# Kernel optimization log

Measured on AMD Instinct MI355X. Metric: run time of the kernel, lower is better.

The kernel has to match this reference:

```python
import jax, jax.numpy as jnp
import numpy as np

T, D, H, E, K = 8192, 512, 1024, 16, 2  # tokens, d_model, d_hidden, num_expert, top_k


def setup_inputs() -> dict:
    key = jax.random.key(0)
    ks = jax.random.split(key, 4)
    return {
        "x": jax.random.normal(ks[0], (T, D), jnp.float32),
        "Wg": jax.random.normal(ks[1], (D, E), jnp.float32) * (D ** -0.5),
        "bg": jnp.zeros((E,), jnp.float32),
        "W1": jax.random.normal(ks[2], (E, D, H), jnp.float32) * (D ** -0.5),
        "b1": jnp.zeros((E, H), jnp.float32),
        "W2": jax.random.normal(ks[3], (E, H, D), jnp.float32) * (H ** -0.5),
        "b2": jnp.zeros((E, D), jnp.float32),
    }


def _moe(x, Wg, bg, W1, b1, W2, b2):
    # NaiveGate: linear -> top-k -> softmax over the k selected logits
    logits = x @ Wg + bg                              # [T, E]
    top_val, top_idx = jax.lax.top_k(logits, K)       # [T, K]
    score = jax.nn.softmax(top_val, axis=-1)          # [T, K]
    # Dispatch + per-expert MLP + combine. Mathematically identical to the
    # scatter/grouped-GEMM/gather: for each expert, the per-token combine
    # weight is the gate score if the token routed there, else 0.
    out = jnp.zeros_like(x)
    for e in range(E):  # fixed small loop over structurally distinct experts
        h = jax.nn.gelu(x @ W1[e] + b1[e], approximate=False)  # [T, H]
        y = h @ W2[e] + b2[e]                                   # [T, D]
        w_e = jnp.sum(jnp.where(top_idx == e, score, 0.0), axis=-1)  # [T]
        out = out + w_e[:, None] * y
    return out


def reference(x, Wg, bg, W1, b1, W2, b2):
    return _moe(x, Wg, bg, W1, b1, W2, b2)
```

## Files before the change

### kernel.cpp

```cpp
#include <hip/hip_runtime.h>
#include <hip/hip_bf16.h>
#include <math.h>

#define TT 8192
#define DD 512
#define HH 1024
#define EE 16
#define NSLOT 18432
#define MAXTILES 144
#define BM 128
#define RETRYCAP 1024

typedef __attribute__((ext_vector_type(8))) short bf16x8;
typedef __attribute__((ext_vector_type(8))) unsigned short u16x8;
typedef __attribute__((ext_vector_type(4))) float f32x4;

__device__ __forceinline__ unsigned short f2bf(float f) {
  union { float f; unsigned u; } v; v.f = f;
  unsigned r = v.u + 0x7fffu + ((v.u >> 16) & 1u);
  return (unsigned short)(r >> 16);
}

__device__ __forceinline__ float bf2f(unsigned short u) {
  union { unsigned u; float f; } v; v.u = ((unsigned)u) << 16;
  return v.f;
}

__device__ __forceinline__ void gload16(const void* g, void* l) {
  __builtin_amdgcn_global_load_lds(
      (const __attribute__((address_space(1))) unsigned int*)g,
      (__attribute__((address_space(3))) unsigned int*)l, 16, 0, 0);
}

__device__ __forceinline__ float gelu_f(float v) {
  float s = fabsf(v) * 0.70710678118654752f;
  float t = 1.0f / (1.0f + 0.3275911f * s);
  float poly = t * (0.254829592f +
              t * (-0.284496736f +
              t * (1.421413741f +
              t * (-1.453152027f +
              t * 1.061405429f))));
  float erfa = 1.0f - poly * __expf(-s * s);
  float erfv = (v >= 0.f) ? erfa : -erfa;
  return 0.5f * v * (1.0f + erfv);
}

__device__ __forceinline__ int tile_decode(const int* __restrict__ counts,
                                           int mt, int* e_out, int* row0_out) {
  int off = 0, rem = mt;
#pragma unroll
  for (int q = 0; q < EE; q++) {
    int tl = (counts[q] + BM - 1) / BM;
    if (rem < tl) { *e_out = q; *row0_out = off + rem * BM; return 1; }
    rem -= tl;
    off += tl * BM;
  }
  return 0;
}

__global__ __launch_bounds__(256) void transpose_cv_kernel(
    const float* __restrict__ W1, const float* __restrict__ W2,
    unsigned short* __restrict__ w1t, unsigned short* __restrict__ w2t) {
  __shared__ unsigned short t[64][68];
  int bid = blockIdx.x;
  int tid = threadIdx.x;
  const float* src;
  unsigned short* dst;
  int R, C, c0, r0;
  if (bid < 2048) {
    int cx = bid & 15, ry = (bid >> 4) & 7, mat = bid >> 7;
    src = W1 + (size_t)mat * DD * HH; dst = w1t + (size_t)mat * DD * HH;
    R = DD; C = HH; c0 = cx * 64; r0 = ry * 64;
  } else {
    int b = bid - 2048;
    int cx = b & 7, ry = (b >> 3) & 15, mat = b >> 7;
    src = W2 + (size_t)mat * DD * HH; dst = w2t + (size_t)mat * DD * HH;
    R = HH; C = DD; c0 = cx * 64; r0 = ry * 64;
  }
#pragma unroll
  for (int p = 0; p < 4; p++) {
    int r = tid >> 2;
    int c4 = (tid & 3) + p * 4;
    float4 v = *(const float4*)(src + (size_t)(r0 + r) * C + c0 + c4 * 4);
    t[c4 * 4 + 0][r] = f2bf(v.x);
    t[c4 * 4 + 1][r] = f2bf(v.y);
    t[c4 * 4 + 2][r] = f2bf(v.z);
    t[c4 * 4 + 3][r] = f2bf(v.w);
  }
  __syncthreads();
#pragma unroll
  for (int p = 0; p < 4; p++) {
    int oc = (tid >> 4) + p * 16;
    int ch = tid & 15;
    ushort4 v = *(ushort4*)(&t[oc][ch * 4]);
    *(ushort4*)(dst + (size_t)(c0 + oc) * R + r0 + ch * 4) = v;
  }
}

__global__ __launch_bounds__(256) void gate_mfma_kernel(
    const float* __restrict__ x, const float* __restrict__ Wg,
    const float* __restrict__ bg, unsigned short* __restrict__ xb,
    int* __restrict__ gate_e, float* __restrict__ gate_w,
    int* __restrict__ counts, int* __restrict__ nretry,
    int* __restrict__ retry) {
  __shared__ __align__(16) unsigned short As[128][40];
  __shared__ int cnt_s[EE];
  int tid = threadIdx.x;
  int lane = tid & 63;
  int wave = tid >> 6;
  int tok0 = blockIdx.x * 128;
  if (tid < EE) cnt_s[tid] = 0;
  int e = lane & 15;
  int kb = (lane >> 4) * 8;
  bf16x8 bfrag[16];
#pragma unroll
  for (int ks = 0; ks < 16; ks++) {
    int kbase = ks * 32 + kb;
#pragma unroll
    for (int j = 0; j < 8; j++)
      bfrag[ks][j] = (short)f2bf(Wg[(kbase + j) * EE + e]);
  }
  float bge = bg[e];
  f32x4 acc[2];
  {
    f32x4 z = {0.f, 0.f, 0.f, 0.f};
    acc[0] = z; acc[1] = z;
  }
  int srow = tid >> 1;
  int sc0 = (tid & 1) * 16;
  const float* xrow = x + (size_t)(tok0 + srow) * DD + sc0;
  unsigned short* xbrow = xb + (size_t)(tok0 + srow) * DD + sc0;
  for (int ks = 0; ks < 16; ks++) {
    int k0 = ks * 32;
    __syncthreads();
    float4 v0 = *(const float4*)(xrow + k0);
    float4 v1 = *(const float4*)(xrow + k0 + 4);
    float4 v2 = *(const float4*)(xrow + k0 + 8);
    float4 v3 = *(const float4*)(xrow + k0 + 12);
    u16x8 w0, w1;
    w0[0] = f2bf(v0.x); w0[1] = f2bf(v0.y); w0[2] = f2bf(v0.z); w0[3] = f2bf(v0.w);
    w0[4] = f2bf(v1.x); w0[5] = f2bf(v1.y); w0[6] = f2bf(v1.z); w0[7] = f2bf(v1.w);
    w1[0] = f2bf(v2.x); w1[1] = f2bf(v2.y); w1[2] = f2bf(v2.z); w1[3] = f2bf(v2.w);
    w1[4] = f2bf(v3.x); w1[5] = f2bf(v3.y); w1[6] = f2bf(v3.z); w1[7] = f2bf(v3.w);
    *(u16x8*)(xbrow + k0) = w0;
    *(u16x8*)(xbrow + k0 + 8) = w1;
    *(u16x8*)(&As[srow][sc0]) = w0;
    *(u16x8*)(&As[srow][sc0 + 8]) = w1;
    __syncthreads();
    bf16x8 a0 = *(const bf16x8*)(&As[wave * 32 + (lane & 15)][kb]);
    bf16x8 a1 = *(const bf16x8*)(&As[wave * 32 + 16 + (lane & 15)][kb]);
    acc[0] = __builtin_amdgcn_mfma_f32_16x16x32_bf16(a0, bfrag[ks], acc[0], 0, 0, 0);
    acc[1] = __builtin_amdgcn_mfma_f32_16x16x32_bf16(a1, bfrag[ks], acc[1], 0, 0, 0);
  }
#pragma unroll
  for (int m = 0; m < 2; m++) {
#pragma unroll
    for (int r = 0; r < 4; r++) {
      float lf = acc[m][r] + bge;
      float v1 = -1e30f, v2 = -1e30f, v3 = -1e30f;
      int i1 = 0, i2 = 0;
#pragma unroll
      for (int q = 0; q < EE; q++) {
        float v = __shfl(lf, (lane & 48) | q);
        if (v > v1) { v3 = v2; v2 = v1; i2 = i1; v1 = v; i1 = q; }
        else if (v > v2) { v3 = v2; v2 = v; i2 = q; }
        else if (v > v3) { v3 = v; }
      }
      if ((lane & 15) == 0) {
        int t2 = tok0 + wave * 32 + m * 16 + ((lane >> 4) << 2) + r;
        float p = expf(v2 - v1);
        float s = 1.0f / (1.0f + p);
        gate_e[t2 * 2] = i1;
        gate_e[t2 * 2 + 1] = i2;
        gate_w[t2 * 2] = s;
        gate_w[t2 * 2 + 1] = p * s;
        atomicAdd(&cnt_s[i1], 1);
        atomicAdd(&cnt_s[i2], 1);
        if (v2 - v3 < 0.02f) {
          int pos = atomicAdd(nretry, 1);
          if (pos < RETRYCAP) retry[pos] = t2;
        }
      }
    }
  }
  __syncthreads();
  if (tid < EE) atomicAdd(&counts[tid], cnt_s[tid]);
}

__global__ __launch_bounds__(256) void gatefix_kernel(
    const float* __restrict__ x, const float* __restrict__ Wg,
    const float* __restrict__ bg, const int* __restrict__ nretry,
    const int* __restrict__ retry, int* __restrict__ gate_e,
    float* __restrict__ gate_w, int* __restrict__ counts) {
  __shared__ float lg[16][17];
  __shared__ int toks[16];
  int tid = threadIdx.x;
  int sl = tid >> 4, e = tid & 15;
  int s = blockIdx.x * 16 + sl;
  int n = *nretry; if (n > RETRYCAP) n = RETRYCAP;
  int active = (s < n);
  int tok = 0;
  if (active) tok = retry[s];
  if (active) {
    const float* xr = x + (size_t)tok * DD;
    double a0 = 0.0, a1 = 0.0, a2 = 0.0, a3 = 0.0;
    for (int i = 0; i < DD / 4; i++) {
      a0 += (double)xr[i * 4 + 0] * (double)Wg[(i * 4 + 0) * EE + e];
      a1 += (double)xr[i * 4 + 1] * (double)Wg[(i * 4 + 1) * EE + e];
      a2 += (double)xr[i * 4 + 2] * (double)Wg[(i * 4 + 2) * EE + e];
      a3 += (double)xr[i * 4 + 3] * (double)Wg[(i * 4 + 3) * EE + e];
    }
    double acc = (a0 + a1) + (a2 + a3);
    lg[sl][e] = (float)(acc + (double)bg[e]);
    toks[sl] = tok;
  }
  __syncthreads();
  if (active && e == 0) {
    float v1 = -1e30f, v2 = -1e30f;
    int i1 = 0, i2 = 0;
#pragma unroll
    for (int q = 0; q < EE; q++) {
      float v = lg[sl][q];
      if (v > v1) { v2 = v1; i2 = i1; v1 = v; i1 = q; }
      else if (v > v2) { v2 = v; i2 = q; }
    }
    int t2 = toks[sl];
    int o1 = gate_e[t2 * 2], o2 = gate_e[t2 * 2 + 1];
    float p = expf(v2 - v1);
    float sc = 1.0f / (1.0f + p);
    gate_e[t2 * 2] = i1;
    gate_e[t2 * 2 + 1] = i2;
    gate_w[t2 * 2] = sc;
    gate_w[t2 * 2 + 1] = p * sc;
    if (o1 != i1 || o2 != i2) {
      atomicSub(&counts[o1], 1);
      atomicSub(&counts[o2], 1);
      atomicAdd(&counts[i1], 1);
      atomicAdd(&counts[i2], 1);
    }
  }
}

__global__ __launch_bounds__(256) void scatter_kernel(
    const int* __restrict__ gate_e, const float* __restrict__ gate_w,
    const int* __restrict__ counts, int* __restrict__ fill,
    int* __restrict__ slot_token, float* __restrict__ slot_w,
    int* __restrict__ slot_of) {
  __shared__ int lcnt[EE];
  __shared__ int lbase[EE];
  __shared__ int offs_s[EE];
  int tid = threadIdx.x;
  int t = blockIdx.x * 256 + tid;
  if (tid < EE) lcnt[tid] = 0;
  if (tid == 0) {
    int off = 0;
    for (int q = 0; q < EE; q++) {
      offs_s[q] = off;
      off += ((counts[q] + BM - 1) / BM) * BM;
    }
  }
  __syncthreads();
  int e0 = gate_e[t * 2], e1 = gate_e[t * 2 + 1];
  int p0 = atomicAdd(&lcnt[e0], 1);
  int p1 = atomicAdd(&lcnt[e1], 1);
  __syncthreads();
  if (tid < EE) lbase[tid] = atomicAdd(&fill[tid], lcnt[tid]);
  __syncthreads();
  int s0 = offs_s[e0] + lbase[e0] + p0;
  int s1 = offs_s[e1] + lbase[e1] + p1;
  slot_token[s0] = t;
  slot_w[s0] = gate_w[t * 2];
  slot_of[t * 2] = s0;
  slot_token[s1] = t;
  slot_w[s1] = gate_w[t * 2 + 1];
  slot_of[t * 2 + 1] = s1;
}

__global__ __launch_bounds__(256) void gemm1_kernel(
    const unsigned short* __restrict__ xb, const unsigned short* __restrict__ w1t,
    const float* __restrict__ b1, const int* __restrict__ slot_token,
    const int* __restrict__ counts, unsigned short* __restrict__ hb) {
  int e, row0;
  if (!tile_decode(counts, blockIdx.y, &e, &row0)) return;
  int n0 = blockIdx.x * 128;
  __shared__ unsigned short As[3][128][32];
  __shared__ unsigned short Bs[3][128][32];
  int tid = threadIdx.x;
  int lane = tid & 63;
  int wave = tid >> 6;
  int wm = wave >> 1, wn = wave & 1;
  int ra = tid >> 2, c = tid & 3;
  int tok_a = slot_token[row0 + ra]; if (tok_a < 0) tok_a = 0;
  int tok_b = slot_token[row0 + ra + 64]; if (tok_b < 0) tok_b = 0;
  const unsigned short* wbase = w1t + ((size_t)e * HH * DD);
  const unsigned short* gA0 = xb + (size_t)tok_a * DD + c * 8;
  const unsigned short* gA1 = xb + (size_t)tok_b * DD + c * 8;
  const unsigned short* gB0 = wbase + (size_t)(n0 + ra) * DD + c * 8;
  const unsigned short* gB1 = wbase + (size_t)(n0 + ra + 64) * DD + c * 8;
  f32x4 acc[4][4];
#pragma unroll
  for (int m = 0; m < 4; m++)
#pragma unroll
    for (int n = 0; n < 4; n++) {
      f32x4 z = {0.f, 0.f, 0.f, 0.f};
      acc[m][n] = z;
    }
  const int NK = DD / 32;
#pragma unroll
  for (int p = 0; p < 2; p++) {
    int kj = p * 32;
    gload16(gA0 + kj, &As[p][ra][c * 8]);
    gload16(gA1 + kj, &As[p][ra + 64][c * 8]);
    gload16(gB0 + kj, &Bs[p][ra][c * 8]);
    gload16(gB1 + kj, &Bs[p][ra + 64][c * 8]);
  }
  for (int kk = 0; kk < NK; kk++) {
    int cur = kk % 3;
    if (kk + 2 < NK) {
      int k2 = (kk + 2) * 32;
      int nx = (kk + 2) % 3;
      gload16(gA0 + k2, &As[nx][ra][c * 8]);
      gload16(gA1 + k2, &As[nx][ra + 64][c * 8]);
      gload16(gB0 + k2, &Bs[nx][ra][c * 8]);
      gload16(gB1 + k2, &Bs[nx][ra + 64][c * 8]);
      asm volatile("s_waitcnt vmcnt(8)" ::: "memory");
    } else if (kk + 1 < NK) {
      asm volatile("s_waitcnt vmcnt(4)" ::: "memory");
    } else {
      asm volatile("s_waitcnt vmcnt(0)" ::: "memory");
    }
    __builtin_amdgcn_s_barrier();
    bf16x8 a[4], b[4];
#pragma unroll
    for (int m = 0; m < 4; m++)
      a[m] = *(const bf16x8*)(&As[cur][wm * 64 + m * 16 + (lane & 15)][(lane >> 4) * 8]);
#pragma unroll
    for (int n = 0; n < 4; n++)
      b[n] = *(const bf16x8*)(&Bs[cur][wn * 64 + n * 16 + (lane & 15)][(lane >> 4) * 8]);
#pragma unroll
    for (int m = 0; m < 4; m++)
#pragma unroll
      for (int n = 0; n < 4; n++)
        acc[m][n] = __builtin_amdgcn_mfma_f32_16x16x32_bf16(a[m], b[n], acc[m][n], 0, 0, 0);
    asm volatile("" ::: "memory");
    __builtin_amdgcn_s_barrier();
  }
  const float* b1e = b1 + (size_t)e * HH;
#pragma unroll
  for (int m = 0; m < 4; m++) {
#pragma unroll
    for (int r = 0; r < 4; r++) {
      int slot = row0 + wm * 64 + m * 16 + ((lane >> 4) << 2) + r;
      unsigned short* hrow = hb + (size_t)slot * HH;
#pragma unroll
      for (int n = 0; n < 4; n++) {
        int hc = n0 + wn * 64 + n * 16 + (lane & 15);
        float v = acc[m][n][r] + b1e[hc];
        hrow[hc] = f2bf(gelu_f(v));
      }
    }
  }
}

template <int USE_Y>
__global__ __launch_bounds__(256) void gemm2_kernel(
    const unsigned short* __restrict__ hb, const unsigned short* __restrict__ w2t,
    const float* __restrict__ b2, const int* __restrict__ slot_token,
    const float* __restrict__ slot_w, const int* __restrict__ counts,
    unsigned short* __restrict__ yw, float* __restrict__ out) {
  int e, row0;
  if (!tile_decode(counts, blockIdx.y, &e, &row0)) return;
  int n0 = blockIdx.x * 128;
  __shared__ unsigned short As[3][128][32];
  __shared__ unsigned short Bs[3][128][32];
  int tid = threadIdx.x;
  int lane = tid & 63;
  int wave = tid >> 6;
  int wm = wave >> 1, wn = wave & 1;
  int ra = tid >> 2, c = tid & 3;
  const unsigned short* wbase = w2t + ((size_t)e * DD * HH);
  const unsigned short* gA0 = hb + (size_t)(row0 + ra) * HH + c * 8;
  const unsigned short* gA1 = hb + (size_t)(row0 + ra + 64) * HH + c * 8;
  const unsigned short* gB0 = wbase + (size_t)(n0 + ra) * HH + c * 8;
  const unsigned short* gB1 = wbase + (size_t)(n0 + ra + 64) * HH + c * 8;
  f32x4 acc[4][4];
#pragma unroll
  for (int m = 0; m < 4; m++)
#pragma unroll
    for (int n = 0; n < 4; n++) {
      f32x4 z = {0.f, 0.f, 0.f, 0.f};
      acc[m][n] = z;
    }
  const int NK = HH / 32;
#pragma unroll
  for (int p = 0; p < 2; p++) {
    int kj = p * 32;
    gload16(gA0 + kj, &As[p][ra][c * 8]);
    gload16(gA1 + kj, &As[p][ra + 64][c * 8]);
    gload16(gB0 + kj, &Bs[p][ra][c * 8]);
    gload16(gB1 + kj, &Bs[p][ra + 64][c * 8]);
  }
  for (int kk = 0; kk < NK; kk++) {
    int cur = kk % 3;
    if (kk + 2 < NK) {
      int k2 = (kk + 2) * 32;
      int nx = (kk + 2) % 3;
      gload16(gA0 + k2, &As[nx][ra][c * 8]);
      gload16(gA1 + k2, &As[nx][ra + 64][c * 8]);
      gload16(gB0 + k2, &Bs[nx][ra][c * 8]);
      gload16(gB1 + k2, &Bs[nx][ra + 64][c * 8]);
      asm volatile("s_waitcnt vmcnt(8)" ::: "memory");
    } else if (kk + 1 < NK) {
      asm volatile("s_waitcnt vmcnt(4)" ::: "memory");
    } else {
      asm volatile("s_waitcnt vmcnt(0)" ::: "memory");
    }
    __builtin_amdgcn_s_barrier();
    bf16x8 a[4], b[4];
#pragma unroll
    for (int m = 0; m < 4; m++)
      a[m] = *(const bf16x8*)(&As[cur][wm * 64 + m * 16 + (lane & 15)][(lane >> 4) * 8]);
#pragma unroll
    for (int n = 0; n < 4; n++)
      b[n] = *(const bf16x8*)(&Bs[cur][wn * 64 + n * 16 + (lane & 15)][(lane >> 4) * 8]);
#pragma unroll
    for (int m = 0; m < 4; m++)
#pragma unroll
      for (int n = 0; n < 4; n++)
        acc[m][n] = __builtin_amdgcn_mfma_f32_16x16x32_bf16(a[m], b[n], acc[m][n], 0, 0, 0);
    asm volatile("" ::: "memory");
    __builtin_amdgcn_s_barrier();
  }
  const float* b2e = b2 + (size_t)e * DD;
#pragma unroll
  for (int m = 0; m < 4; m++) {
#pragma unroll
    for (int r = 0; r < 4; r++) {
      int slot = row0 + wm * 64 + m * 16 + ((lane >> 4) << 2) + r;
      if (USE_Y) {
        float w = slot_w[slot];
        unsigned short* yrow = yw + (size_t)slot * DD;
#pragma unroll
        for (int n = 0; n < 4; n++) {
          int dc = n0 + wn * 64 + n * 16 + (lane & 15);
          yrow[dc] = f2bf(w * (acc[m][n][r] + b2e[dc]));
        }
      } else {
        int tok = slot_token[slot];
        if (tok >= 0) {
          float w = slot_w[slot];
          float* orow = out + (size_t)tok * DD;
#pragma unroll
          for (int n = 0; n < 4; n++) {
            int dc = n0 + wn * 64 + n * 16 + (lane & 15);
            float v = acc[m][n][r] + b2e[dc];
            atomicAdd(&orow[dc], w * v);
          }
        }
      }
    }
  }
}

__global__ __launch_bounds__(256) void combine_kernel(
    const unsigned short* __restrict__ yw, const int* __restrict__ slot_of,
    float* __restrict__ out) {
  int gid = blockIdx.x * 256 + threadIdx.x;
  int t = gid >> 6;
  int d0 = (gid & 63) * 8;
  int s1 = slot_of[t * 2], s2 = slot_of[t * 2 + 1];
  const ushort4* p1 = (const ushort4*)(yw + (size_t)s1 * DD + d0);
  const ushort4* p2 = (const ushort4*)(yw + (size_t)s2 * DD + d0);
  ushort4 a0 = p1[0], a1 = p1[1];
  ushort4 b0 = p2[0], b1 = p2[1];
  float4 o0, o1;
  o0.x = bf2f(a0.x) + bf2f(b0.x);
  o0.y = bf2f(a0.y) + bf2f(b0.y);
  o0.z = bf2f(a0.z) + bf2f(b0.z);
  o0.w = bf2f(a0.w) + bf2f(b0.w);
  o1.x = bf2f(a1.x) + bf2f(b1.x);
  o1.y = bf2f(a1.y) + bf2f(b1.y);
  o1.z = bf2f(a1.z) + bf2f(b1.z);
  o1.w = bf2f(a1.w) + bf2f(b1.w);
  float* orow = out + (size_t)t * DD + d0;
  ((float4*)orow)[0] = o0;
  ((float4*)orow)[1] = o1;
}

extern "C" void kernel_launch(void* const* d_in, const int* in_sizes, int n_in,
                              void* d_out, int out_size, void* d_ws, size_t ws_size,
                              hipStream_t stream) {
  const float* x  = (const float*)d_in[0];
  const float* Wg = (const float*)d_in[1];
  const float* bg = (const float*)d_in[2];
  const float* W1 = (const float*)d_in[3];
  const float* b1 = (const float*)d_in[4];
  const float* W2 = (const float*)d_in[5];
  const float* b2 = (const float*)d_in[6];
  float* out = (float*)d_out;

  uint8_t* w = (uint8_t*)d_ws;
  size_t o = 0;
  unsigned short* xb  = (unsigned short*)(w + o); o += (size_t)TT * DD * 2;
  unsigned short* w1t = (unsigned short*)(w + o); o += (size_t)EE * DD * HH * 2;
  unsigned short* w2t = (unsigned short*)(w + o); o += (size_t)EE * DD * HH * 2;
  unsigned short* hb  = (unsigned short*)(w + o); o += (size_t)NSLOT * HH * 2;
  int*   slot_token = (int*)(w + o);   o += (size_t)NSLOT * 4;
  float* slot_w     = (float*)(w + o); o += (size_t)NSLOT * 4;
  int*   slot_of    = (int*)(w + o);   o += (size_t)TT * 2 * 4;
  int*   gate_e     = (int*)(w + o);   o += (size_t)TT * 2 * 4;
  float* gate_w     = (float*)(w + o); o += (size_t)TT * 2 * 4;
  int*   counts     = (int*)(w + o);   o += 64;
  int*   nretry     = (int*)(w + o);   o += 64;
  int*   fill       = (int*)(w + o);   o += 64;
  int*   retry      = (int*)(w + o);   o += RETRYCAP * 4;
  unsigned short* yw = (unsigned short*)(w + o);
  size_t need_y = o + (size_t)NSLOT * DD * 2;
  int use_y = (ws_size >= need_y);

  hipMemsetAsync(counts, 0, 192, stream);
  hipMemsetAsync(slot_token, 0xFF, (size_t)NSLOT * 4, stream);
  if (!use_y) hipMemsetAsync(d_out, 0, (size_t)TT * DD * 4, stream);

  transpose_cv_kernel<<<4096, 256, 0, stream>>>(W1, W2, w1t, w2t);
  gate_mfma_kernel<<<TT / 128, 256, 0, stream>>>(x, Wg, bg, xb, gate_e, gate_w,
                                                 counts, nretry, retry);
  gatefix_kernel<<<RETRYCAP / 16, 256, 0, stream>>>(x, Wg, bg, nretry, retry,
                                                    gate_e, gate_w, counts);
  scatter_kernel<<<TT / 256, 256, 0, stream>>>(gate_e, gate_w, counts, fill,
                                               slot_token, slot_w, slot_of);
  {
    dim3 g(HH / 128, MAXTILES);
    gemm1_kernel<<<g, 256, 0, stream>>>(xb, w1t, b1, slot_token, counts, hb);
  }
  {
    dim3 g(DD / 128, MAXTILES);
    if (use_y)
      gemm2_kernel<1><<<g, 256, 0, stream>>>(hb, w2t, b2, slot_token, slot_w,
                                             counts, yw, out);
    else
      gemm2_kernel<0><<<g, 256, 0, stream>>>(hb, w2t, b2, slot_token, slot_w,
                                             counts, yw, out);
  }
  if (use_y) {
    combine_kernel<<<TT * (DD / 8) / 256, 256, 0, stream>>>(yw, slot_of, out);
  }
}
```

Before: 177.4 us.

## Drop LDS staging in gate kernel and fill only padding slots in scatter

```diff
diff --git a/kernel.cpp b/kernel.cpp
--- a/kernel.cpp
+++ b/kernel.cpp
@@ -97,19 +97,19 @@
   }
 }
 
-__global__ __launch_bounds__(256) void gate_mfma_kernel(
+__global__ __launch_bounds__(128) void gate_mfma_kernel(
     const float* __restrict__ x, const float* __restrict__ Wg,
     const float* __restrict__ bg, unsigned short* __restrict__ xb,
     int* __restrict__ gate_e, float* __restrict__ gate_w,
     int* __restrict__ counts, int* __restrict__ nretry,
     int* __restrict__ retry) {
-  __shared__ __align__(16) unsigned short As[128][40];
   __shared__ int cnt_s[EE];
   int tid = threadIdx.x;
   int lane = tid & 63;
   int wave = tid >> 6;
-  int tok0 = blockIdx.x * 128;
+  int tok0 = blockIdx.x * 32 + wave * 16;
   if (tid < EE) cnt_s[tid] = 0;
+  __syncthreads();
   int e = lane & 15;
   int kb = (lane >> 4) * 8;
   bf16x8 bfrag[16];
@@ -121,65 +121,46 @@
       bfrag[ks][j] = (short)f2bf(Wg[(kbase + j) * EE + e]);
   }
   float bge = bg[e];
-  f32x4 acc[2];
-  {
-    f32x4 z = {0.f, 0.f, 0.f, 0.f};
-    acc[0] = z; acc[1] = z;
-  }
-  int srow = tid >> 1;
-  int sc0 = (tid & 1) * 16;
-  const float* xrow = x + (size_t)(tok0 + srow) * DD + sc0;
-  unsigned short* xbrow = xb + (size_t)(tok0 + srow) * DD + sc0;
+  f32x4 acc = {0.f, 0.f, 0.f, 0.f};
+  const float* xrow = x + (size_t)(tok0 + (lane & 15)) * DD + kb;
+  unsigned short* xbrow = xb + (size_t)(tok0 + (lane & 15)) * DD + kb;
+#pragma unroll 4
   for (int ks = 0; ks < 16; ks++) {
     int k0 = ks * 32;
-    __syncthreads();
     float4 v0 = *(const float4*)(xrow + k0);
     float4 v1 = *(const float4*)(xrow + k0 + 4);
-    float4 v2 = *(const float4*)(xrow + k0 + 8);
-    float4 v3 = *(const float4*)(xrow + k0 + 12);
-    u16x8 w0, w1;
+    u16x8 w0;
     w0[0] = f2bf(v0.x); w0[1] = f2bf(v0.y); w0[2] = f2bf(v0.z); w0[3] = f2bf(v0.w);
     w0[4] = f2bf(v1.x); w0[5] = f2bf(v1.y); w0[6] = f2bf(v1.z); w0[7] = f2bf(v1.w);
-    w1[0] = f2bf(v2.x); w1[1] = f2bf(v2.y); w1[2] = f2bf(v2.z); w1[3] = f2bf(v2.w);
-    w1[4] = f2bf(v3.x); w1[5] = f2bf(v3.y); w1[6] = f2bf(v3.z); w1[7] = f2bf(v3.w);
     *(u16x8*)(xbrow + k0) = w0;
-    *(u16x8*)(xbrow + k0 + 8) = w1;
-    *(u16x8*)(&As[srow][sc0]) = w0;
-    *(u16x8*)(&As[srow][sc0 + 8]) = w1;
-    __syncthreads();
-    bf16x8 a0 = *(const bf16x8*)(&As[wave * 32 + (lane & 15)][kb]);
-    bf16x8 a1 = *(const bf16x8*)(&As[wave * 32 + 16 + (lane & 15)][kb]);
-    acc[0] = __builtin_amdgcn_mfma_f32_16x16x32_bf16(a0, bfrag[ks], acc[0], 0, 0, 0);
-    acc[1] = __builtin_amdgcn_mfma_f32_16x16x32_bf16(a1, bfrag[ks], acc[1], 0, 0, 0);
-  }
-#pragma unroll
-  for (int m = 0; m < 2; m++) {
-#pragma unroll
-    for (int r = 0; r < 4; r++) {
-      float lf = acc[m][r] + bge;
-      float v1 = -1e30f, v2 = -1e30f, v3 = -1e30f;
-      int i1 = 0, i2 = 0;
-#pragma unroll
-      for (int q = 0; q < EE; q++) {
-        float v = __shfl(lf, (lane & 48) | q);
-        if (v > v1) { v3 = v2; v2 = v1; i2 = i1; v1 = v; i1 = q; }
-        else if (v > v2) { v3 = v2; v2 = v; i2 = q; }
-        else if (v > v3) { v3 = v; }
-      }
-      if ((lane & 15) == 0) {
-        int t2 = tok0 + wave * 32 + m * 16 + ((lane >> 4) << 2) + r;
-        float p = expf(v2 - v1);
-        float s = 1.0f / (1.0f + p);
-        gate_e[t2 * 2] = i1;
-        gate_e[t2 * 2 + 1] = i2;
-        gate_w[t2 * 2] = s;
-        gate_w[t2 * 2 + 1] = p * s;
-        atomicAdd(&cnt_s[i1], 1);
-        atomicAdd(&cnt_s[i2], 1);
-        if (v2 - v3 < 0.02f) {
-          int pos = atomicAdd(nretry, 1);
-          if (pos < RETRYCAP) retry[pos] = t2;
-        }
+    union { u16x8 u; bf16x8 b; } cv; cv.u = w0;
+    acc = __builtin_amdgcn_mfma_f32_16x16x32_bf16(cv.b, bfrag[ks], acc, 0, 0, 0);
+  }
+#pragma unroll
+  for (int r = 0; r < 4; r++) {
+    float lf = acc[r] + bge;
+    float v1 = -1e30f, v2 = -1e30f, v3 = -1e30f;
+    int i1 = 0, i2 = 0;
+#pragma unroll
+    for (int q = 0; q < EE; q++) {
+      float v = __shfl(lf, (lane & 48) | q);
+      if (v > v1) { v3 = v2; v2 = v1; i2 = i1; v1 = v; i1 = q; }
+      else if (v > v2) { v3 = v2; v2 = v; i2 = q; }
+      else if (v > v3) { v3 = v; }
+    }
+    if ((lane & 15) == 0) {
+      int t2 = tok0 + ((lane >> 4) << 2) + r;
+      float p = expf(v2 - v1);
+      float s = 1.0f / (1.0f + p);
+      gate_e[t2 * 2] = i1;
+      gate_e[t2 * 2 + 1] = i2;
+      gate_w[t2 * 2] = s;
+      gate_w[t2 * 2 + 1] = p * s;
+      atomicAdd(&cnt_s[i1], 1);
+      atomicAdd(&cnt_s[i2], 1);
+      if (v2 - v3 < 0.02f) {
+        int pos = atomicAdd(nretry, 1);
+        if (pos < RETRYCAP) retry[pos] = t2;
       }
     }
   }
@@ -260,6 +241,15 @@
     }
   }
   __syncthreads();
+  if (blockIdx.x == 0) {
+#pragma unroll
+    for (int q = 0; q < EE; q++) {
+      int cnt = counts[q];
+      int lim = ((cnt + BM - 1) / BM) * BM;
+      for (int p = cnt + tid; p < lim; p += 256)
+        slot_token[offs_s[q] + p] = -1;
+    }
+  }
   int e0 = gate_e[t * 2], e1 = gate_e[t * 2 + 1];
   int p0 = atomicAdd(&lcnt[e0], 1);
   int p1 = atomicAdd(&lcnt[e1], 1);
@@ -519,12 +509,14 @@
   int use_y = (ws_size >= need_y);
 
   hipMemsetAsync(counts, 0, 192, stream);
-  hipMemsetAsync(slot_token, 0xFF, (size_t)NSLOT * 4, stream);
-  if (!use_y) hipMemsetAsync(d_out, 0, (size_t)TT * DD * 4, stream);
+  if (!use_y) {
+    hipMemsetAsync(slot_token, 0xFF, (size_t)NSLOT * 4, stream);
+    hipMemsetAsync(d_out, 0, (size_t)TT * DD * 4, stream);
+  }
 
   transpose_cv_kernel<<<4096, 256, 0, stream>>>(W1, W2, w1t, w2t);
-  gate_mfma_kernel<<<TT / 128, 256, 0, stream>>>(x, Wg, bg, xb, gate_e, gate_w,
-                                                 counts, nretry, retry);
+  gate_mfma_kernel<<<TT / 32, 128, 0, stream>>>(x, Wg, bg, xb, gate_e, gate_w,
+                                                counts, nretry, retry);
   gatefix_kernel<<<RETRYCAP / 16, 256, 0, stream>>>(x, Wg, bg, nretry, retry,
                                                     gate_e, gate_w, counts);
   scatter_kernel<<<TT / 256, 256, 0, stream>>>(gate_e, gate_w, counts, fill,
```

New measurement: 172.5 us. -2.7%, faster.
